# Kernel tuning notes

Hardware: AMD Instinct MI355X
Metric: run time of the kernel (lower is better)

The kernel has to match this reference:

```python
import jax, jax.numpy as jnp
import numpy as np

IN_FEATURES = 4096
OUT_FEATURES = 4096
KERNEL_SIZE = 4  # MaxPool1d stride defaults to kernel_size
SCALE = 0.5


def setup_inputs() -> dict:
    key = jax.random.key(0)
    kx, kw, kb = jax.random.split(key, 3)
    bound = 1.0 / np.sqrt(IN_FEATURES)
    x = jax.random.normal(kx, (4096, IN_FEATURES), dtype=jnp.float32)
    W = jax.random.uniform(kw, (OUT_FEATURES, IN_FEATURES), dtype=jnp.float32, minval=-bound, maxval=bound)
    b = jax.random.uniform(kb, (OUT_FEATURES,), dtype=jnp.float32, minval=-bound, maxval=bound)
    return {"x": x, "W": W, "b": b}


def reference(x, W, b) -> jnp.ndarray:
    # Linear: [B, I] @ [I, O] + [O] -> [B, O]
    y = jnp.einsum("bi,oi->bo", x, W) + b
    B, O = y.shape
    K = KERNEL_SIZE
    n_win = (O - K) // K + 1  # stride == kernel_size, no padding
    # Non-overlapping window max-pool: [B, n_win, K] -> max over K
    pooled = y[:, : n_win * K].reshape(B, n_win, K).max(axis=-1)
    # Sum over pooled dim, then scale -> [B]
    return pooled.sum(axis=-1) * SCALE
```

## Files before the change

kernel.cpp:

```cpp
#include <hip/hip_runtime.h>
#include <hip/hip_bf16.h>

#define KDIM 4096
#define NKT 128
#define NELEM16 (1u << 24)

typedef float f32x4 __attribute__((ext_vector_type(4)));
typedef short bf16x8 __attribute__((ext_vector_type(8)));

typedef const __attribute__((address_space(1))) unsigned int g_u32;
typedef __attribute__((address_space(3))) unsigned int l_u32;

__device__ __forceinline__ void gload_lds16(const void* g, void* l) {
    __builtin_amdgcn_global_load_lds((g_u32*)g, (l_u32*)l, 16, 0, 0);
}

__device__ __forceinline__ unsigned int pack_bf16x2(float lo, float hi) {
    __hip_bfloat162 h = __float22bfloat162_rn(float2{lo, hi});
    union { __hip_bfloat162 h; unsigned int u; } c; c.h = h; return c.u;
}

__global__ __launch_bounds__(256)
void pack3(const float* __restrict__ x, const float* __restrict__ W,
           unsigned short* __restrict__ xb, unsigned short* __restrict__ wb)
{
    const unsigned int stride = gridDim.x * blockDim.x;
    for (unsigned int i = blockIdx.x * blockDim.x + threadIdx.x; i < (1u << 22); i += stride) {
        const float* __restrict__ in;
        unsigned short* __restrict__ out;
        unsigned int row, col, j;
        if (i < (1u << 21)) {
            j = i;
            const unsigned int cp = j & 3;
            const unsigned int rl = (j >> 2) & 255;
            const unsigned int kt = (j >> 10) & 127;
            const unsigned int mt = j >> 17;
            row = mt * 256 + rl;
            col = kt * 32 + (cp ^ (rl & 3)) * 8;
            in = x; out = xb;
        } else {
            j = i - (1u << 21);
            const unsigned int cp = j & 3;
            const unsigned int rl = (j >> 2) & 127;
            const unsigned int kt = (j >> 9) & 127;
            const unsigned int nt = j >> 16;
            row = nt * 128 + rl;
            col = kt * 32 + (cp ^ (rl & 3)) * 8;
            in = W; out = wb;
        }
        const float4* sp = (const float4*)(in + (size_t)row * KDIM + col);
        const float4 a = sp[0], b = sp[1];
        uint4 o;
        o.x = pack_bf16x2(a.x, a.y); o.y = pack_bf16x2(a.z, a.w);
        o.z = pack_bf16x2(b.x, b.y); o.w = pack_bf16x2(b.z, b.w);
        *(uint4*)(out + (size_t)j * 8) = o;
    }
}

#define STAGE3(kt, BUFE)                                                        \
    {                                                                           \
        const unsigned short* ga = Abase + (size_t)(kt) * 8192 + wid * 1024 + lane * 8; \
        gload_lds16(ga,       &lds[(BUFE) + wid * 1024]);                       \
        gload_lds16(ga + 512, &lds[(BUFE) + wid * 1024 + 512]);                 \
        const unsigned short* gb = Bbase + (size_t)(kt) * 4096 + wid * 512 + lane * 8;  \
        gload_lds16(gb,       &lds[(BUFE) + 8192 + wid * 512]);                 \
    }

#define READ_AB(BUFE)                                                           \
    _Pragma("unroll") for (int mf = 0; mf < 4; ++mf)                            \
        afr[mf] = *(const bf16x8*)&lds[(BUFE) + rdA + mf * 512];                \
    _Pragma("unroll") for (int nf = 0; nf < 4; ++nf)                            \
        bfr[nf] = *(const bf16x8*)&lds[(BUFE) + rdB + nf * 512];

#define MFMA16()                                                                \
    __builtin_amdgcn_s_setprio(1);                                              \
    _Pragma("unroll") for (int mf = 0; mf < 4; ++mf)                            \
      _Pragma("unroll") for (int nf = 0; nf < 4; ++nf)                          \
        acc[mf][nf] = __builtin_amdgcn_mfma_f32_16x16x32_bf16(                  \
            afr[mf], bfr[nf], acc[mf][nf], 0, 0, 0);                            \
    __builtin_amdgcn_s_setprio(0);

#define PHASE(t, BUFE, STGE, VMW)                                               \
    {                                                                           \
        READ_AB(BUFE);                                                          \
        MFMA16();                                                               \
        if ((t) + 2 < NKT) STAGE3((t) + 2, STGE);                               \
        VMW;                                                                    \
        __builtin_amdgcn_s_barrier();                                           \
        __builtin_amdgcn_sched_barrier(0);                                      \
    }

#define VM3 asm volatile("s_waitcnt vmcnt(3)" ::: "memory")
#define VM0 asm volatile("s_waitcnt vmcnt(0)" ::: "memory")

__global__ __launch_bounds__(512, 4)
void gemm_cores(const unsigned short* __restrict__ A,
                const unsigned short* __restrict__ B,
                const float* __restrict__ bias,
                float* __restrict__ out)
{
    __shared__ unsigned short lds[36864];

    const int tid  = threadIdx.x;
    const int lane = tid & 63;
    const int wid  = tid >> 6;
    const int wm   = wid >> 1;
    const int wn   = wid & 1;
    const int c15  = lane & 15;
    const int q4   = lane >> 4;

    const int bid = blockIdx.x;
    const int wg  = (bid & 7) * 64 + (bid >> 3);
    const int bm  = wg >> 5;
    const int bn  = wg & 31;

    const unsigned short* Abase = A + ((size_t)bm << 20);
    const unsigned short* Bbase = B + ((size_t)bn << 19);

    const int swz = ((q4 ^ (c15 & 3)) * 8);
    const int rdA = (wm * 64 + c15) * 32 + swz;
    const int rdB = 8192 + (wn * 64 + c15) * 32 + swz;

    f32x4 acc[4][4];
    #pragma unroll
    for (int i = 0; i < 4; ++i)
        #pragma unroll
        for (int j = 0; j < 4; ++j)
            acc[i][j] = (f32x4)0.0f;

    bf16x8 afr[4], bfr[4];

    STAGE3(0, 0);
    STAGE3(1, 12288);
    VM3;
    __builtin_amdgcn_s_barrier();
    __builtin_amdgcn_sched_barrier(0);

    for (int tt = 0; tt < 126; tt += 3) {
        PHASE(tt,     0,     24576, VM3);
        PHASE(tt + 1, 12288, 0,     VM3);
        PHASE(tt + 2, 24576, 12288, VM3);
    }
    PHASE(126, 0, 24576, VM0);
    READ_AB(12288);
    MFMA16();

    float rs[4][4];
    #pragma unroll
    for (int mf = 0; mf < 4; ++mf)
        #pragma unroll
        for (int r = 0; r < 4; ++r)
            rs[mf][r] = 0.0f;

    #pragma unroll
    for (int nf = 0; nf < 4; ++nf) {
        const float bv = bias[bn * 128 + wn * 64 + nf * 16 + c15];
        #pragma unroll
        for (int mf = 0; mf < 4; ++mf) {
            #pragma unroll
            for (int r = 0; r < 4; ++r) {
                float v = acc[mf][nf][r] + bv;
                v = fmaxf(v, __shfl_xor(v, 1));
                v = fmaxf(v, __shfl_xor(v, 2));
                v += __shfl_xor(v, 4);
                v += __shfl_xor(v, 8);
                rs[mf][r] += v;
            }
        }
    }

    if (c15 == 0) {
        #pragma unroll
        for (int mf = 0; mf < 4; ++mf)
            #pragma unroll
            for (int r = 0; r < 4; ++r) {
                const int row = bm * 256 + wm * 64 + mf * 16 + q4 * 4 + r;
                atomicAdd(&out[row], 0.5f * rs[mf][r]);
            }
    }
}

__global__ __launch_bounds__(256, 2)
void fused_gemm_pool_fallback(const float* __restrict__ x,
                              const float* __restrict__ W,
                              const float* __restrict__ b,
                              float* __restrict__ out)
{
    __shared__ unsigned short As[128][72];
    __shared__ unsigned short Bs[128][72];

    const int tid  = threadIdx.x;
    const int lane = tid & 63;
    const int wid  = tid >> 6;
    const int wm   = wid >> 1;
    const int wn   = wid & 1;

    const int bid = blockIdx.x;
    const int wg  = (bid & 7) * 128 + (bid >> 3);
    const int bm  = wg >> 5;
    const int bn  = wg & 31;

    const int srow = tid >> 4;
    const int scol = tid & 15;

    const float* xbase = x + (size_t)(bm * 128 + srow) * KDIM + scol * 4;
    const float* wbase = W + (size_t)(bn * 128 + srow) * KDIM + scol * 4;

    f32x4 acc[4][4];
    #pragma unroll
    for (int i = 0; i < 4; ++i)
        #pragma unroll
        for (int j = 0; j < 4; ++j)
            acc[i][j] = (f32x4)0.0f;

    float4 ra[8], rb[8];
    #pragma unroll
    for (int p = 0; p < 8; ++p) {
        ra[p] = *(const float4*)(xbase + (size_t)(p * 16) * KDIM);
        rb[p] = *(const float4*)(wbase + (size_t)(p * 16) * KDIM);
    }

    for (int kt = 0; kt < KDIM / 64; ++kt) {
        #pragma unroll
        for (int p = 0; p < 8; ++p) {
            const int r = srow + p * 16;
            uint2 pa, pb;
            pa.x = pack_bf16x2(ra[p].x, ra[p].y);
            pa.y = pack_bf16x2(ra[p].z, ra[p].w);
            pb.x = pack_bf16x2(rb[p].x, rb[p].y);
            pb.y = pack_bf16x2(rb[p].z, rb[p].w);
            *(uint2*)&As[r][scol * 4] = pa;
            *(uint2*)&Bs[r][scol * 4] = pb;
        }
        __syncthreads();

        if (kt + 1 < KDIM / 64) {
            const float* xa = xbase + (size_t)(kt + 1) * 64;
            const float* wa = wbase + (size_t)(kt + 1) * 64;
            #pragma unroll
            for (int p = 0; p < 8; ++p) {
                ra[p] = *(const float4*)(xa + (size_t)(p * 16) * KDIM);
                rb[p] = *(const float4*)(wa + (size_t)(p * 16) * KDIM);
            }
        }

        #pragma unroll
        for (int k0 = 0; k0 < 2; ++k0) {
            const int kk = k0 * 32 + (lane >> 4) * 8;
            bf16x8 af[4], bfr[4];
            #pragma unroll
            for (int mf = 0; mf < 4; ++mf)
                af[mf] = *(const bf16x8*)&As[wm * 64 + mf * 16 + (lane & 15)][kk];
            #pragma unroll
            for (int nf = 0; nf < 4; ++nf)
                bfr[nf] = *(const bf16x8*)&Bs[wn * 64 + nf * 16 + (lane & 15)][kk];
            #pragma unroll
            for (int mf = 0; mf < 4; ++mf)
                #pragma unroll
                for (int nf = 0; nf < 4; ++nf)
                    acc[mf][nf] = __builtin_amdgcn_mfma_f32_16x16x32_bf16(
                        af[mf], bfr[nf], acc[mf][nf], 0, 0, 0);
        }
        __syncthreads();
    }

    float rs[4][4];
    #pragma unroll
    for (int mf = 0; mf < 4; ++mf)
        #pragma unroll
        for (int r = 0; r < 4; ++r)
            rs[mf][r] = 0.0f;

    #pragma unroll
    for (int nf = 0; nf < 4; ++nf) {
        const float bv = b[bn * 128 + wn * 64 + nf * 16 + (lane & 15)];
        #pragma unroll
        for (int mf = 0; mf < 4; ++mf) {
            #pragma unroll
            for (int r = 0; r < 4; ++r) {
                float v = acc[mf][nf][r] + bv;
                v = fmaxf(v, __shfl_xor(v, 1));
                v = fmaxf(v, __shfl_xor(v, 2));
                v += __shfl_xor(v, 4);
                v += __shfl_xor(v, 8);
                rs[mf][r] += v;
            }
        }
    }

    if ((lane & 15) == 0) {
        #pragma unroll
        for (int mf = 0; mf < 4; ++mf)
            #pragma unroll
            for (int r = 0; r < 4; ++r) {
                const int row = bm * 128 + wm * 64 + mf * 16 + (lane >> 4) * 4 + r;
                atomicAdd(&out[row], 0.5f * rs[mf][r]);
            }
    }
}

extern "C" void kernel_launch(void* const* d_in, const int* in_sizes, int n_in,
                              void* d_out, int out_size, void* d_ws, size_t ws_size,
                              hipStream_t stream) {
    const float* x = (const float*)d_in[0];
    const float* W = (const float*)d_in[1];
    const float* b = (const float*)d_in[2];
    float* out = (float*)d_out;

    hipMemsetAsync(out, 0, (size_t)out_size * sizeof(float), stream);

    const size_t need = (size_t)NELEM16 * 2 * sizeof(unsigned short);
    if (ws_size >= need) {
        unsigned short* xb = (unsigned short*)d_ws;
        unsigned short* wb = xb + (size_t)NELEM16;
        pack3<<<dim3(2048), dim3(256), 0, stream>>>(x, W, xb, wb);
        gemm_cores<<<dim3(512), dim3(512), 0, stream>>>(xb, wb, b, out);
    } else {
        fused_gemm_pool_fallback<<<dim3(1024), dim3(256), 0, stream>>>(x, W, b, out);
    }
}
```

Before: 175.3 us.

## Load B fragments directly from global into registers, shrink LDS staging

The W operand is now packed in MFMA fragment order so each wave reads its B fragments straight from global memory into double-buffered registers one k-step ahead, instead of staging B through LDS. Only A goes through the LDS triple buffer, which cuts LDS footprint and LDS read traffic, and the A swizzle is changed to a different XOR pattern. The two waves sharing wn now each fetch the same B data from global/L2 separately, and register pressure rises from holding two B fragment sets.

```diff
diff --git a/kernel.cpp b/kernel.cpp
--- a/kernel.cpp
+++ b/kernel.cpp
@@ -21,7 +21,7 @@
 }
 
 __global__ __launch_bounds__(256)
-void pack3(const float* __restrict__ x, const float* __restrict__ W,
+void pack4(const float* __restrict__ x, const float* __restrict__ W,
            unsigned short* __restrict__ xb, unsigned short* __restrict__ wb)
 {
     const unsigned int stride = gridDim.x * blockDim.x;
@@ -36,16 +36,16 @@
             const unsigned int kt = (j >> 10) & 127;
             const unsigned int mt = j >> 17;
             row = mt * 256 + rl;
-            col = kt * 32 + (cp ^ (rl & 3)) * 8;
+            col = kt * 32 + (cp ^ ((rl >> 1) & 3)) * 8;
             in = x; out = xb;
         } else {
             j = i - (1u << 21);
-            const unsigned int cp = j & 3;
-            const unsigned int rl = (j >> 2) & 127;
-            const unsigned int kt = (j >> 9) & 127;
-            const unsigned int nt = j >> 16;
-            row = nt * 128 + rl;
-            col = kt * 32 + (cp ^ (rl & 3)) * 8;
+            const unsigned int lane = j & 63;
+            const unsigned int nf   = (j >> 6) & 7;
+            const unsigned int kt   = (j >> 9) & 127;
+            const unsigned int nt   = j >> 16;
+            row = nt * 128 + nf * 16 + (lane & 15);
+            col = kt * 32 + (lane >> 4) * 8;
             in = W; out = wb;
         }
         const float4* sp = (const float4*)(in + (size_t)row * KDIM + col);
@@ -62,35 +62,36 @@
         const unsigned short* ga = Abase + (size_t)(kt) * 8192 + wid * 1024 + lane * 8; \
         gload_lds16(ga,       &lds[(BUFE) + wid * 1024]);                       \
         gload_lds16(ga + 512, &lds[(BUFE) + wid * 1024 + 512]);                 \
-        const unsigned short* gb = Bbase + (size_t)(kt) * 4096 + wid * 512 + lane * 8;  \
-        gload_lds16(gb,       &lds[(BUFE) + 8192 + wid * 512]);                 \
-    }
-
-#define READ_AB(BUFE)                                                           \
+    }
+
+#define READ_A(BUFE)                                                            \
     _Pragma("unroll") for (int mf = 0; mf < 4; ++mf)                            \
-        afr[mf] = *(const bf16x8*)&lds[(BUFE) + rdA + mf * 512];                \
-    _Pragma("unroll") for (int nf = 0; nf < 4; ++nf)                            \
-        bfr[nf] = *(const bf16x8*)&lds[(BUFE) + rdB + nf * 512];
-
-#define MFMA16()                                                                \
+        afr[mf] = *(const bf16x8*)&lds[(BUFE) + rdA + mf * 512];
+
+#define LOAD_B(dst, t)                                                          \
+    _Pragma("unroll") for (int n = 0; n < 4; ++n)                               \
+        dst[n] = *(const bf16x8*)&Bb[(size_t)(t) * 4096 + (wn * 4 + n) * 512 + lane * 8];
+
+#define MFMA16(BC)                                                              \
     __builtin_amdgcn_s_setprio(1);                                              \
     _Pragma("unroll") for (int mf = 0; mf < 4; ++mf)                            \
       _Pragma("unroll") for (int nf = 0; nf < 4; ++nf)                          \
         acc[mf][nf] = __builtin_amdgcn_mfma_f32_16x16x32_bf16(                  \
-            afr[mf], bfr[nf], acc[mf][nf], 0, 0, 0);                            \
+            afr[mf], BC[nf], acc[mf][nf], 0, 0, 0);                             \
     __builtin_amdgcn_s_setprio(0);
 
-#define PHASE(t, BUFE, STGE, VMW)                                               \
+#define PHASE(t, BUFE, STGE, BCUR, BNXT, VMW)                                   \
     {                                                                           \
-        READ_AB(BUFE);                                                          \
-        MFMA16();                                                               \
+        READ_A(BUFE);                                                           \
+        if ((t) + 1 < NKT) LOAD_B(BNXT, (t) + 1);                               \
         if ((t) + 2 < NKT) STAGE3((t) + 2, STGE);                               \
+        MFMA16(BCUR);                                                           \
         VMW;                                                                    \
         __builtin_amdgcn_s_barrier();                                           \
         __builtin_amdgcn_sched_barrier(0);                                      \
     }
 
-#define VM3 asm volatile("s_waitcnt vmcnt(3)" ::: "memory")
+#define VM6 asm volatile("s_waitcnt vmcnt(6)" ::: "memory")
 #define VM0 asm volatile("s_waitcnt vmcnt(0)" ::: "memory")
 
 __global__ __launch_bounds__(512, 4)
@@ -99,7 +100,7 @@
                 const float* __restrict__ bias,
                 float* __restrict__ out)
 {
-    __shared__ unsigned short lds[36864];
+    __shared__ unsigned short lds[24576];
 
     const int tid  = threadIdx.x;
     const int lane = tid & 63;
@@ -115,11 +116,9 @@
     const int bn  = wg & 31;
 
     const unsigned short* Abase = A + ((size_t)bm << 20);
-    const unsigned short* Bbase = B + ((size_t)bn << 19);
-
-    const int swz = ((q4 ^ (c15 & 3)) * 8);
-    const int rdA = (wm * 64 + c15) * 32 + swz;
-    const int rdB = 8192 + (wn * 64 + c15) * 32 + swz;
+    const unsigned short* Bb    = B + ((size_t)bn << 19);
+
+    const int rdA = (wm * 64 + c15) * 32 + ((q4 ^ ((c15 >> 1) & 3)) * 8);
 
     f32x4 acc[4][4];
     #pragma unroll
@@ -128,22 +127,27 @@
         for (int j = 0; j < 4; ++j)
             acc[i][j] = (f32x4)0.0f;
 
-    bf16x8 afr[4], bfr[4];
+    bf16x8 afr[4];
+    bf16x8 bE[4], bO[4];
 
     STAGE3(0, 0);
-    STAGE3(1, 12288);
-    VM3;
+    STAGE3(1, 8192);
+    LOAD_B(bE, 0);
+    VM6;
     __builtin_amdgcn_s_barrier();
     __builtin_amdgcn_sched_barrier(0);
 
-    for (int tt = 0; tt < 126; tt += 3) {
-        PHASE(tt,     0,     24576, VM3);
-        PHASE(tt + 1, 12288, 0,     VM3);
-        PHASE(tt + 2, 24576, 12288, VM3);
-    }
-    PHASE(126, 0, 24576, VM0);
-    READ_AB(12288);
-    MFMA16();
+    for (int tt = 0; tt < 126; tt += 6) {
+        PHASE(tt + 0, 0,     16384, bE, bO, VM6);
+        PHASE(tt + 1, 8192,  0,     bO, bE, VM6);
+        PHASE(tt + 2, 16384, 8192,  bE, bO, VM6);
+        PHASE(tt + 3, 0,     16384, bO, bE, VM6);
+        PHASE(tt + 4, 8192,  0,     bE, bO, VM6);
+        PHASE(tt + 5, 16384, 8192,  bO, bE, VM6);
+    }
+    PHASE(126, 0, 16384, bE, bO, VM0);
+    READ_A(8192);
+    MFMA16(bO);
 
     float rs[4][4];
     #pragma unroll
@@ -313,7 +317,7 @@
     if (ws_size >= need) {
         unsigned short* xb = (unsigned short*)d_ws;
         unsigned short* wb = xb + (size_t)NELEM16;
-        pack3<<<dim3(2048), dim3(256), 0, stream>>>(x, W, xb, wb);
+        pack4<<<dim3(2048), dim3(256), 0, stream>>>(x, W, xb, wb);
         gemm_cores<<<dim3(512), dim3(512), 0, stream>>>(xb, wb, b, out);
     } else {
         fused_gemm_pool_fallback<<<dim3(1024), dim3(256), 0, stream>>>(x, W, b, out);
```

Measured after the change: 213.2 us. +21.6%, slower.
